# Kernel tuning notes

Hardware: AMD Instinct MI355X
Metric: run time of the kernel (lower is better)

Reference implementation:

```python
import jax, jax.numpy as jnp
import numpy as np
from jax import lax

EPS = 1e-5

def _sign(x):
    # sign with sign(0)=+1, as used in XNOR-style binarization
    return jnp.where(x >= 0, 1.0, -1.0).astype(x.dtype)

def binarize(x):
    # straight-through estimator: forward = sign(x), backward = identity
    return x + lax.stop_gradient(_sign(x) - x)

def batchnorm(x, p):
    # p: [4, C] rows = (gamma, beta, running_mean, running_var); eval-mode BN
    g, b, m, v = p[0], p[1], p[2], p[3]
    shape = (1, -1) + (1,) * (x.ndim - 2)
    inv = g / jnp.sqrt(v + EPS)
    return (x - m.reshape(shape)) * inv.reshape(shape) + b.reshape(shape)

def conv2d(x, w):
    return lax.conv_general_dilated(x, w, window_strides=(1, 1), padding='VALID',
                                    dimension_numbers=('NCHW', 'OIHW', 'NCHW'))

def maxpool2(x):
    return lax.reduce_window(x, -jnp.inf, lax.max, (1, 1, 2, 2), (1, 1, 2, 2), 'VALID')

def hardtanh(x):
    return jnp.clip(x, -1.0, 1.0)


def setup_inputs() -> dict:
    key = jax.random.key(0)
    ks = jax.random.split(key, 16)
    B = 16384
    x = jax.random.normal(ks[0], (B, 3, 22, 22), jnp.float32)
    w1 = jax.random.normal(ks[1], (32, 3, 3, 3), jnp.float32) * 0.1
    w2 = jax.random.normal(ks[2], (32, 32, 3, 3), jnp.float32) * 0.1
    w3 = jax.random.normal(ks[3], (64, 32, 3, 3), jnp.float32) * 0.1
    w_fc1 = jax.random.normal(ks[4], (128, 64), jnp.float32) * 0.1
    w_fc2 = jax.random.normal(ks[5], (2, 128), jnp.float32) * 0.1
    w_fc3 = jax.random.normal(ks[6], (4, 128), jnp.float32) * 0.1

    def make_bn(k, c):
        k1, k2, k3, k4 = jax.random.split(k, 4)
        gamma = jax.random.uniform(k1, (c,), jnp.float32, 0.5, 1.5)
        beta = jax.random.normal(k2, (c,), jnp.float32) * 0.1
        mean = jax.random.normal(k3, (c,), jnp.float32) * 0.1
        var = jax.random.uniform(k4, (c,), jnp.float32, 0.5, 1.5)
        return jnp.stack([gamma, beta, mean, var])  # [4, C]

    bn1 = make_bn(ks[7], 32)
    bn2 = make_bn(ks[8], 32)
    bn3 = make_bn(ks[9], 64)
    bn4 = make_bn(ks[10], 128)
    bn5 = make_bn(ks[11], 2)
    bn6 = make_bn(ks[12], 4)
    return {'x': x, 'w1': w1, 'w2': w2, 'w3': w3, 'w_fc1': w_fc1, 'w_fc2': w_fc2,
            'w_fc3': w_fc3, 'bn1': bn1, 'bn2': bn2, 'bn3': bn3, 'bn4': bn4,
            'bn5': bn5, 'bn6': bn6}


def reference(x, w1, w2, w3, w_fc1, w_fc2, w_fc3, bn1, bn2, bn3, bn4, bn5, bn6):
    # binary=True, binarize_input=True, bitwidth=input_bitwidth=1:
    # every BinarizeConv2d/BinarizeLinear binarizes both its input and weights.
    h = hardtanh(batchnorm(conv2d(binarize(x), binarize(w1)), bn1))   # [B,32,20,20]
    h = maxpool2(h)                                                    # [B,32,10,10]
    h = hardtanh(batchnorm(conv2d(binarize(h), binarize(w2)), bn2))   # [B,32,8,8]
    h = maxpool2(h)                                                    # [B,32,4,4]
    h = hardtanh(batchnorm(conv2d(binarize(h), binarize(w3)), bn3))   # [B,64,2,2]
    h = maxpool2(h)                                                    # [B,64,1,1]
    h = h.reshape(-1, 64)                                              # [B,64]
    h = hardtanh(batchnorm(binarize(h) @ binarize(w_fc1).T, bn4))      # [B,128]
    out1 = jax.nn.softmax(batchnorm(h @ w_fc2.T, bn5), axis=1)         # [B,2]
    out2 = batchnorm(h @ w_fc3.T, bn6)                                 # [B,4]
    return (out1, out2)
```

## Files before the change

kernel.cpp:

```cpp
#include <hip/hip_runtime.h>
#include <cstdint>
#include <cmath>

#define OFF_W1   0
#define OFF_T1   32
#define OFF_W2   64
#define OFF_T2   352
#define OFF_W3   384
#define OFF_T3   960
#define OFF_WFC1 1024
#define OFF_A4   1280
#define OFF_C4   1408
#define OFF_WF2  1536
#define OFF_WF3  1792
#define OFF_BN5  2304
#define OFF_BN6  2308

__device__ __forceinline__ int thr_int(double nterms, double g, double b, double m, double v) {
    double inv = g / sqrt(v + 1e-5);
    double t = m - b / inv;
    double thr = floor((nterms - t) * 0.5);
    if (thr < -2147000000.0) thr = -2147000000.0;
    if (thr >  2147000000.0) thr =  2147000000.0;
    return (int)thr;
}

__global__ void k_prep(const float* __restrict__ w1, const float* __restrict__ w2,
                       const float* __restrict__ w3, const float* __restrict__ wfc1,
                       const float* __restrict__ wfc2, const float* __restrict__ wfc3,
                       const float* __restrict__ bn1, const float* __restrict__ bn2,
                       const float* __restrict__ bn3, const float* __restrict__ bn4,
                       const float* __restrict__ bn5, const float* __restrict__ bn6,
                       unsigned int* __restrict__ ws) {
    int t = threadIdx.x;
    float* wsf = (float*)ws;
    int*   wsi = (int*)ws;
    if (t < 32) {
        unsigned int bits = 0;
        for (int j = 0; j < 27; ++j) bits |= (w1[t*27+j] >= 0.f ? 1u : 0u) << j;
        ws[OFF_W1 + t] = bits;
        wsi[OFF_T1 + t] = thr_int(27.0,  bn1[t], bn1[32+t], bn1[64+t], bn1[96+t]);
        wsi[OFF_T2 + t] = thr_int(288.0, bn2[t], bn2[32+t], bn2[64+t], bn2[96+t]);
    }
    for (int idx = t; idx < 288; idx += 256) {
        int o = idx / 9, k = idx - o*9;
        unsigned int bits = 0;
        for (int i = 0; i < 32; ++i) bits |= (w2[(o*32+i)*9 + k] >= 0.f ? 1u : 0u) << i;
        ws[OFF_W2 + idx] = bits;
    }
    for (int idx = t; idx < 576; idx += 256) {
        int o = idx / 9, k = idx - o*9;
        unsigned int bits = 0;
        for (int i = 0; i < 32; ++i) bits |= (w3[(o*32+i)*9 + k] >= 0.f ? 1u : 0u) << i;
        ws[OFF_W3 + idx] = bits;
    }
    if (t < 64) wsi[OFF_T3 + t] = thr_int(288.0, bn3[t], bn3[64+t], bn3[128+t], bn3[192+t]);
    if (t < 128) {
        unsigned int lo = 0, hi = 0;
        for (int j = 0; j < 32; ++j) lo |= (wfc1[t*64+j]    >= 0.f ? 1u : 0u) << j;
        for (int j = 0; j < 32; ++j) hi |= (wfc1[t*64+32+j] >= 0.f ? 1u : 0u) << j;
        ws[OFF_WFC1 + 2*t]     = lo;
        ws[OFF_WFC1 + 2*t + 1] = hi;
        float g = bn4[t], b = bn4[128+t], m = bn4[256+t], v = bn4[384+t];
        float inv = g / sqrtf(v + 1e-5f);
        wsf[OFF_A4 + t] = -2.f * inv;
        wsf[OFF_C4 + t] = (64.f - m) * inv + b;
    }
    for (int idx = t; idx < 256; idx += 256) wsf[OFF_WF2 + idx] = wfc2[idx];
    for (int idx = t; idx < 512; idx += 256) wsf[OFF_WF3 + idx] = wfc3[idx];
    if (t < 2) {
        float g = bn5[t], b = bn5[2+t], m = bn5[4+t], v = bn5[6+t];
        float inv = g / sqrtf(v + 1e-5f);
        wsf[OFF_BN5 + t]     = inv;
        wsf[OFF_BN5 + 2 + t] = b - m * inv;
    }
    if (t < 4) {
        float g = bn6[t], b = bn6[4+t], m = bn6[8+t], v = bn6[12+t];
        float inv = g / sqrtf(v + 1e-5f);
        wsf[OFF_BN6 + t]     = inv;
        wsf[OFF_BN6 + 4 + t] = b - m * inv;
    }
}

__global__ __launch_bounds__(64) void k_main(const float* __restrict__ x,
                                             const unsigned int* __restrict__ ws,
                                             float* __restrict__ out, int B) {
    __shared__ unsigned int s_inrow[66];
    __shared__ unsigned int s_c1[400];
    __shared__ unsigned int s_b1[100];
    __shared__ unsigned int s_b2[16];
    __shared__ float        s_h[128];

    const int tid = threadIdx.x;
    const int b   = blockIdx.x;
    const float* wsf = (const float*)ws;
    const int*   wsi = (const int*)ws;

    for (int r = tid; r < 66; r += 64) {
        int c = r / 22, y = r - c*22;
        const float2* p = (const float2*)(x + ((size_t)b*3 + c)*484 + (size_t)y*22);
        unsigned int bits = 0;
        #pragma unroll
        for (int j = 0; j < 11; ++j) {
            float2 v = p[j];
            bits |= (v.x >= 0.f ? 1u : 0u) << (2*j);
            bits |= (v.y >= 0.f ? 1u : 0u) << (2*j+1);
        }
        s_inrow[r] = bits;
    }
    __syncthreads();

    for (int pos = tid; pos < 400; pos += 64) {
        int y = pos / 20, xx = pos - y*20;
        unsigned int g = 0;
        #pragma unroll
        for (int c = 0; c < 3; ++c)
            #pragma unroll
            for (int dy = 0; dy < 3; ++dy)
                g |= ((s_inrow[c*22 + y + dy] >> xx) & 7u) << (c*9 + dy*3);
        unsigned int word = 0;
        for (int o = 0; o < 32; ++o) {
            int pc = __popc(g ^ ws[OFF_W1 + o]);
            word |= (pc <= wsi[OFF_T1 + o] ? 1u : 0u) << o;
        }
        s_c1[pos] = word;
    }
    __syncthreads();

    for (int p = tid; p < 100; p += 64) {
        int py = p / 10, px = p - py*10;
        int base = (2*py)*20 + 2*px;
        s_b1[p] = s_c1[base] | s_c1[base+1] | s_c1[base+20] | s_c1[base+21];
    }
    __syncthreads();

    {
        int y = tid >> 3, xx = tid & 7;
        unsigned int in9[9];
        #pragma unroll
        for (int dy = 0; dy < 3; ++dy)
            #pragma unroll
            for (int dx = 0; dx < 3; ++dx)
                in9[dy*3+dx] = s_b1[(y+dy)*10 + xx + dx];
        unsigned int word = 0;
        for (int o = 0; o < 32; ++o) {
            int s = 0;
            #pragma unroll
            for (int k = 0; k < 9; ++k)
                s += __popc(in9[k] ^ ws[OFF_W2 + o*9 + k]);
            word |= (s <= wsi[OFF_T2 + o] ? 1u : 0u) << o;
        }
        word |= __shfl_xor(word, 1);
        word |= __shfl_xor(word, 8);
        if ((tid & 9) == 0)
            s_b2[(y>>1)*4 + (xx>>1)] = word;
    }
    __syncthreads();

    unsigned long long b3;
    {
        unsigned int bb[16];
        #pragma unroll
        for (int i = 0; i < 16; ++i) bb[i] = s_b2[i];
        unsigned int w3r[9];
        #pragma unroll
        for (int k = 0; k < 9; ++k) w3r[k] = ws[OFF_W3 + tid*9 + k];
        int thr = wsi[OFF_T3 + tid];
        int anybit = 0;
        #pragma unroll
        for (int py = 0; py < 2; ++py)
            #pragma unroll
            for (int px = 0; px < 2; ++px) {
                int s = 0;
                #pragma unroll
                for (int dy = 0; dy < 3; ++dy)
                    #pragma unroll
                    for (int dx = 0; dx < 3; ++dx)
                        s += __popc(bb[(py+dy)*4 + px + dx] ^ w3r[dy*3+dx]);
                anybit |= (s <= thr) ? 1 : 0;
            }
        b3 = __ballot(anybit);
    }

    {
        const unsigned long long* wfc1b = (const unsigned long long*)(ws + OFF_WFC1);
        for (int j = tid; j < 128; j += 64) {
            int pc = __popcll(b3 ^ wfc1b[j]);
            float pre = fmaf((float)pc, wsf[OFF_A4 + j], wsf[OFF_C4 + j]);
            s_h[j] = fminf(1.f, fmaxf(-1.f, pre));
        }
    }
    __syncthreads();

    {
        float h0 = s_h[tid], h1 = s_h[tid + 64];
        float part[6];
        #pragma unroll
        for (int j = 0; j < 2; ++j)
            part[j] = h0 * wsf[OFF_WF2 + j*128 + tid] + h1 * wsf[OFF_WF2 + j*128 + 64 + tid];
        #pragma unroll
        for (int j = 0; j < 4; ++j)
            part[2+j] = h0 * wsf[OFF_WF3 + j*128 + tid] + h1 * wsf[OFF_WF3 + j*128 + 64 + tid];
        for (int off = 32; off; off >>= 1) {
            #pragma unroll
            for (int j = 0; j < 6; ++j)
                part[j] += __shfl_xor(part[j], off);
        }
        if (tid < 6) {
            if (tid < 2) {
                float y0 = part[0]*wsf[OFF_BN5+0] + wsf[OFF_BN5+2];
                float y1 = part[1]*wsf[OFF_BN5+1] + wsf[OFF_BN5+3];
                float mx = fmaxf(y0, y1);
                float e0 = expf(y0 - mx), e1 = expf(y1 - mx);
                float r  = 1.f / (e0 + e1);
                out[(size_t)b*2 + tid] = (tid == 0 ? e0 : e1) * r;
            } else {
                int j = tid - 2;
                out[(size_t)B*2 + (size_t)b*4 + j] = part[2+j]*wsf[OFF_BN6+j] + wsf[OFF_BN6+4+j];
            }
        }
    }
}

extern "C" void kernel_launch(void* const* d_in, const int* in_sizes, int n_in,
                              void* d_out, int out_size, void* d_ws, size_t ws_size,
                              hipStream_t stream) {
    const float* x    = (const float*)d_in[0];
    const float* w1   = (const float*)d_in[1];
    const float* w2   = (const float*)d_in[2];
    const float* w3   = (const float*)d_in[3];
    const float* wfc1 = (const float*)d_in[4];
    const float* wfc2 = (const float*)d_in[5];
    const float* wfc3 = (const float*)d_in[6];
    const float* bn1  = (const float*)d_in[7];
    const float* bn2  = (const float*)d_in[8];
    const float* bn3  = (const float*)d_in[9];
    const float* bn4  = (const float*)d_in[10];
    const float* bn5  = (const float*)d_in[11];
    const float* bn6  = (const float*)d_in[12];
    unsigned int* ws  = (unsigned int*)d_ws;
    float* out        = (float*)d_out;
    int B = in_sizes[0] / 1452;

    k_prep<<<1, 256, 0, stream>>>(w1, w2, w3, wfc1, wfc2, wfc3,
                                  bn1, bn2, bn3, bn4, bn5, bn6, ws);
    k_main<<<B, 64, 0, stream>>>(x, ws, out, B);
}
```

Measured before the change: 209.4 us.

## Pack four samples per block and parallelize weight prep across blocks

The main kernel now runs four wavefronts per 256-thread block, one sample each, with per-wave shared-memory slices instead of one 64-thread block per sample. This cuts the block count fourfold and is meant to lower launch and scheduling overhead. The prep kernel is split across five blocks that stage the weights into shared memory with coalesced loads before binarizing, replacing strided global reads from a single block. Several inner loops are also fully unrolled. In exchange, block-wide barriers now couple four independent samples, and the final block carries an inactive-wave guard.

```diff
diff --git a/kernel.cpp b/kernel.cpp
--- a/kernel.cpp
+++ b/kernel.cpp
@@ -32,117 +32,153 @@
                        const float* __restrict__ bn3, const float* __restrict__ bn4,
                        const float* __restrict__ bn5, const float* __restrict__ bn6,
                        unsigned int* __restrict__ ws) {
+    __shared__ float stage[9216];
     int t = threadIdx.x;
+    int blk = blockIdx.x;
     float* wsf = (float*)ws;
     int*   wsi = (int*)ws;
-    if (t < 32) {
-        unsigned int bits = 0;
-        for (int j = 0; j < 27; ++j) bits |= (w1[t*27+j] >= 0.f ? 1u : 0u) << j;
-        ws[OFF_W1 + t] = bits;
-        wsi[OFF_T1 + t] = thr_int(27.0,  bn1[t], bn1[32+t], bn1[64+t], bn1[96+t]);
-        wsi[OFF_T2 + t] = thr_int(288.0, bn2[t], bn2[32+t], bn2[64+t], bn2[96+t]);
-    }
-    for (int idx = t; idx < 288; idx += 256) {
-        int o = idx / 9, k = idx - o*9;
-        unsigned int bits = 0;
-        for (int i = 0; i < 32; ++i) bits |= (w2[(o*32+i)*9 + k] >= 0.f ? 1u : 0u) << i;
-        ws[OFF_W2 + idx] = bits;
-    }
-    for (int idx = t; idx < 576; idx += 256) {
-        int o = idx / 9, k = idx - o*9;
-        unsigned int bits = 0;
-        for (int i = 0; i < 32; ++i) bits |= (w3[(o*32+i)*9 + k] >= 0.f ? 1u : 0u) << i;
-        ws[OFF_W3 + idx] = bits;
-    }
-    if (t < 64) wsi[OFF_T3 + t] = thr_int(288.0, bn3[t], bn3[64+t], bn3[128+t], bn3[192+t]);
-    if (t < 128) {
-        unsigned int lo = 0, hi = 0;
-        for (int j = 0; j < 32; ++j) lo |= (wfc1[t*64+j]    >= 0.f ? 1u : 0u) << j;
-        for (int j = 0; j < 32; ++j) hi |= (wfc1[t*64+32+j] >= 0.f ? 1u : 0u) << j;
-        ws[OFF_WFC1 + 2*t]     = lo;
-        ws[OFF_WFC1 + 2*t + 1] = hi;
-        float g = bn4[t], b = bn4[128+t], m = bn4[256+t], v = bn4[384+t];
-        float inv = g / sqrtf(v + 1e-5f);
-        wsf[OFF_A4 + t] = -2.f * inv;
-        wsf[OFF_C4 + t] = (64.f - m) * inv + b;
-    }
-    for (int idx = t; idx < 256; idx += 256) wsf[OFF_WF2 + idx] = wfc2[idx];
-    for (int idx = t; idx < 512; idx += 256) wsf[OFF_WF3 + idx] = wfc3[idx];
-    if (t < 2) {
-        float g = bn5[t], b = bn5[2+t], m = bn5[4+t], v = bn5[6+t];
-        float inv = g / sqrtf(v + 1e-5f);
-        wsf[OFF_BN5 + t]     = inv;
-        wsf[OFF_BN5 + 2 + t] = b - m * inv;
-    }
-    if (t < 4) {
-        float g = bn6[t], b = bn6[4+t], m = bn6[8+t], v = bn6[12+t];
-        float inv = g / sqrtf(v + 1e-5f);
-        wsf[OFF_BN6 + t]     = inv;
-        wsf[OFF_BN6 + 4 + t] = b - m * inv;
-    }
-}
-
-__global__ __launch_bounds__(64) void k_main(const float* __restrict__ x,
-                                             const unsigned int* __restrict__ ws,
-                                             float* __restrict__ out, int B) {
-    __shared__ unsigned int s_inrow[66];
-    __shared__ unsigned int s_c1[400];
-    __shared__ unsigned int s_b1[100];
-    __shared__ unsigned int s_b2[16];
-    __shared__ float        s_h[128];
-
-    const int tid = threadIdx.x;
-    const int b   = blockIdx.x;
+
+    if (blk == 0) {
+        for (int i = t; i < 864; i += 256) stage[i] = w1[i];
+        __syncthreads();
+        if (t < 32) {
+            unsigned int bits = 0;
+            for (int j = 0; j < 27; ++j) bits |= (stage[t*27+j] >= 0.f ? 1u : 0u) << j;
+            ws[OFF_W1 + t] = bits;
+            wsi[OFF_T1 + t] = thr_int(27.0,  bn1[t], bn1[32+t], bn1[64+t], bn1[96+t]);
+            wsi[OFF_T2 + t] = thr_int(288.0, bn2[t], bn2[32+t], bn2[64+t], bn2[96+t]);
+        }
+        for (int i = t; i < 256; i += 256) wsf[OFF_WF2 + i] = wfc2[i];
+        for (int i = t; i < 512; i += 256) wsf[OFF_WF3 + i] = wfc3[i];
+        if (t < 2) {
+            float g = bn5[t], b = bn5[2+t], m = bn5[4+t], v = bn5[6+t];
+            float inv = g / sqrtf(v + 1e-5f);
+            wsf[OFF_BN5 + t]     = inv;
+            wsf[OFF_BN5 + 2 + t] = b - m * inv;
+        }
+        if (t >= 4 && t < 8) {
+            int j = t - 4;
+            float g = bn6[j], b = bn6[4+j], m = bn6[8+j], v = bn6[12+j];
+            float inv = g / sqrtf(v + 1e-5f);
+            wsf[OFF_BN6 + j]     = inv;
+            wsf[OFF_BN6 + 4 + j] = b - m * inv;
+        }
+    } else if (blk == 1) {
+        for (int i = t; i < 9216; i += 256) stage[i] = w2[i];
+        __syncthreads();
+        for (int idx = t; idx < 288; idx += 256) {
+            int o = idx / 9, k = idx - o*9;
+            unsigned int bits = 0;
+            for (int i = 0; i < 32; ++i)
+                bits |= (stage[(o*32+i)*9 + k] >= 0.f ? 1u : 0u) << i;
+            ws[OFF_W2 + idx] = bits;
+        }
+    } else if (blk == 2 || blk == 3) {
+        int base = (blk - 2) * 9216;
+        for (int i = t; i < 9216; i += 256) stage[i] = w3[base + i];
+        __syncthreads();
+        for (int idx = t; idx < 288; idx += 256) {
+            int o = idx / 9, k = idx - o*9;
+            unsigned int bits = 0;
+            for (int i = 0; i < 32; ++i)
+                bits |= (stage[(o*32+i)*9 + k] >= 0.f ? 1u : 0u) << i;
+            ws[OFF_W3 + base/32 + idx] = bits;
+        }
+    } else {
+        for (int i = t; i < 8192; i += 256) stage[i] = wfc1[i];
+        __syncthreads();
+        if (t < 128) {
+            unsigned int lo = 0, hi = 0;
+            for (int j = 0; j < 32; ++j) lo |= (stage[t*64+j]    >= 0.f ? 1u : 0u) << j;
+            for (int j = 0; j < 32; ++j) hi |= (stage[t*64+32+j] >= 0.f ? 1u : 0u) << j;
+            ws[OFF_WFC1 + 2*t]     = lo;
+            ws[OFF_WFC1 + 2*t + 1] = hi;
+            float g = bn4[t], b = bn4[128+t], m = bn4[256+t], v = bn4[384+t];
+            float inv = g / sqrtf(v + 1e-5f);
+            wsf[OFF_A4 + t] = -2.f * inv;
+            wsf[OFF_C4 + t] = (64.f - m) * inv + b;
+        }
+        if (t >= 128 && t < 192) {
+            int j = t - 128;
+            wsi[OFF_T3 + j] = thr_int(288.0, bn3[j], bn3[64+j], bn3[128+j], bn3[192+j]);
+        }
+    }
+}
+
+#define WSTRIDE 712
+__global__ __launch_bounds__(256) void k_main(const float* __restrict__ x,
+                                              const unsigned int* __restrict__ ws,
+                                              float* __restrict__ out, int B) {
+    __shared__ unsigned int s_u[4 * WSTRIDE];
+
+    const int tid = threadIdx.x & 63;
+    const int wid = threadIdx.x >> 6;
+    const int b   = blockIdx.x * 4 + wid;
+    const bool act = (b < B);
     const float* wsf = (const float*)ws;
     const int*   wsi = (const int*)ws;
 
-    for (int r = tid; r < 66; r += 64) {
-        int c = r / 22, y = r - c*22;
-        const float2* p = (const float2*)(x + ((size_t)b*3 + c)*484 + (size_t)y*22);
-        unsigned int bits = 0;
-        #pragma unroll
-        for (int j = 0; j < 11; ++j) {
-            float2 v = p[j];
-            bits |= (v.x >= 0.f ? 1u : 0u) << (2*j);
-            bits |= (v.y >= 0.f ? 1u : 0u) << (2*j+1);
-        }
-        s_inrow[r] = bits;
-    }
-    __syncthreads();
-
-    for (int pos = tid; pos < 400; pos += 64) {
-        int y = pos / 20, xx = pos - y*20;
-        unsigned int g = 0;
-        #pragma unroll
-        for (int c = 0; c < 3; ++c)
-            #pragma unroll
-            for (int dy = 0; dy < 3; ++dy)
-                g |= ((s_inrow[c*22 + y + dy] >> xx) & 7u) << (c*9 + dy*3);
-        unsigned int word = 0;
-        for (int o = 0; o < 32; ++o) {
-            int pc = __popc(g ^ ws[OFF_W1 + o]);
-            word |= (pc <= wsi[OFF_T1 + o] ? 1u : 0u) << o;
-        }
-        s_c1[pos] = word;
-    }
-    __syncthreads();
-
-    for (int p = tid; p < 100; p += 64) {
-        int py = p / 10, px = p - py*10;
-        int base = (2*py)*20 + 2*px;
-        s_b1[p] = s_c1[base] | s_c1[base+1] | s_c1[base+20] | s_c1[base+21];
-    }
-    __syncthreads();
-
-    {
+    unsigned int* inrow = s_u + wid * WSTRIDE;
+    unsigned int* c1    = inrow + 66;
+    unsigned int* pb1   = c1 + 400;
+    unsigned int* pb2   = pb1 + 100;
+    float*        hbuf  = (float*)(pb2 + 16);
+
+    if (act) {
+        for (int r = tid; r < 66; r += 64) {
+            int c = r / 22, y = r - c*22;
+            const float2* p = (const float2*)(x + ((size_t)b*3 + c)*484 + (size_t)y*22);
+            unsigned int bits = 0;
+            #pragma unroll
+            for (int j = 0; j < 11; ++j) {
+                float2 v = p[j];
+                bits |= (v.x >= 0.f ? 1u : 0u) << (2*j);
+                bits |= (v.y >= 0.f ? 1u : 0u) << (2*j+1);
+            }
+            inrow[r] = bits;
+        }
+    }
+    __syncthreads();
+
+    if (act) {
+        for (int pos = tid; pos < 400; pos += 64) {
+            int y = pos / 20, xx = pos - y*20;
+            unsigned int g = 0;
+            #pragma unroll
+            for (int c = 0; c < 3; ++c)
+                #pragma unroll
+                for (int dy = 0; dy < 3; ++dy)
+                    g |= ((inrow[c*22 + y + dy] >> xx) & 7u) << (c*9 + dy*3);
+            unsigned int word = 0;
+            #pragma unroll
+            for (int o = 0; o < 32; ++o) {
+                int pc = __popc(g ^ ws[OFF_W1 + o]);
+                word |= (pc <= wsi[OFF_T1 + o] ? 1u : 0u) << o;
+            }
+            c1[pos] = word;
+        }
+    }
+    __syncthreads();
+
+    if (act) {
+        for (int p = tid; p < 100; p += 64) {
+            int py = p / 10, px = p - py*10;
+            int base = (2*py)*20 + 2*px;
+            pb1[p] = c1[base] | c1[base+1] | c1[base+20] | c1[base+21];
+        }
+    }
+    __syncthreads();
+
+    if (act) {
         int y = tid >> 3, xx = tid & 7;
         unsigned int in9[9];
         #pragma unroll
         for (int dy = 0; dy < 3; ++dy)
             #pragma unroll
             for (int dx = 0; dx < 3; ++dx)
-                in9[dy*3+dx] = s_b1[(y+dy)*10 + xx + dx];
+                in9[dy*3+dx] = pb1[(y+dy)*10 + xx + dx];
         unsigned int word = 0;
+        #pragma unroll
         for (int o = 0; o < 32; ++o) {
             int s = 0;
             #pragma unroll
@@ -153,15 +189,15 @@
         word |= __shfl_xor(word, 1);
         word |= __shfl_xor(word, 8);
         if ((tid & 9) == 0)
-            s_b2[(y>>1)*4 + (xx>>1)] = word;
-    }
-    __syncthreads();
-
-    unsigned long long b3;
-    {
+            pb2[(y>>1)*4 + (xx>>1)] = word;
+    }
+    __syncthreads();
+
+    unsigned long long b3 = 0;
+    if (act) {
         unsigned int bb[16];
         #pragma unroll
-        for (int i = 0; i < 16; ++i) bb[i] = s_b2[i];
+        for (int i = 0; i < 16; ++i) bb[i] = pb2[i];
         unsigned int w3r[9];
         #pragma unroll
         for (int k = 0; k < 9; ++k) w3r[k] = ws[OFF_W3 + tid*9 + k];
@@ -182,18 +218,18 @@
         b3 = __ballot(anybit);
     }
 
-    {
+    if (act) {
         const unsigned long long* wfc1b = (const unsigned long long*)(ws + OFF_WFC1);
         for (int j = tid; j < 128; j += 64) {
             int pc = __popcll(b3 ^ wfc1b[j]);
             float pre = fmaf((float)pc, wsf[OFF_A4 + j], wsf[OFF_C4 + j]);
-            s_h[j] = fminf(1.f, fmaxf(-1.f, pre));
-        }
-    }
-    __syncthreads();
-
-    {
-        float h0 = s_h[tid], h1 = s_h[tid + 64];
+            hbuf[j] = fminf(1.f, fmaxf(-1.f, pre));
+        }
+    }
+    __syncthreads();
+
+    if (act) {
+        float h0 = hbuf[tid], h1 = hbuf[tid + 64];
         float part[6];
         #pragma unroll
         for (int j = 0; j < 2; ++j)
@@ -201,6 +237,7 @@
         #pragma unroll
         for (int j = 0; j < 4; ++j)
             part[2+j] = h0 * wsf[OFF_WF3 + j*128 + tid] + h1 * wsf[OFF_WF3 + j*128 + 64 + tid];
+        #pragma unroll
         for (int off = 32; off; off >>= 1) {
             #pragma unroll
             for (int j = 0; j < 6; ++j)
@@ -242,7 +279,7 @@
     float* out        = (float*)d_out;
     int B = in_sizes[0] / 1452;
 
-    k_prep<<<1, 256, 0, stream>>>(w1, w2, w3, wfc1, wfc2, wfc3,
+    k_prep<<<5, 256, 0, stream>>>(w1, w2, w3, wfc1, wfc2, wfc3,
                                   bn1, bn2, bn3, bn4, bn5, bn6, ws);
-    k_main<<<B, 64, 0, stream>>>(x, ws, out, B);
-}
+    k_main<<<(B + 3) / 4, 256, 0, stream>>>(x, ws, out, B);
+}
```

After: 203.7 us. 2.7% less time.
